# Kernel tuning notes

Hardware: AMD Instinct MI355X
Metric: run time of the kernel (lower is better)

## Reference

```python
import jax, jax.numpy as jnp
import numpy as np

B, N, DIM, HEADS, DIM_HEAD = 2, 2048, 1024, 16, 64
SCALE = DIM_HEAD ** -0.5


def setup_inputs() -> dict:
    key = jax.random.key(0)
    k1, k2, k3, k4, k5 = jax.random.split(key, 5)
    x = jax.random.normal(k1, (B, N, DIM), dtype=jnp.float32)
    causal_boundary_indices = jax.random.randint(k2, (B,), 0, N)
    # Parameters
    Wq = jax.random.normal(k3, (HEADS, DIM, DIM_HEAD), dtype=jnp.float32) * (DIM ** -0.5)
    Wkv = jax.random.normal(k4, (DIM, 2 * DIM_HEAD), dtype=jnp.float32) * (DIM ** -0.5)
    Wo = jax.random.normal(k5, (HEADS * DIM_HEAD, DIM), dtype=jnp.float32) * ((HEADS * DIM_HEAD) ** -0.5)
    return {"x": x, "Wq": Wq, "Wkv": Wkv, "Wo": Wo,
            "causal_boundary_indices": causal_boundary_indices}


def reference(x, Wq, Wkv, Wo, causal_boundary_indices):
    b, n, d = x.shape
    # Multi-query attention: per-head Q, single shared K/V head
    q = jnp.einsum('bnd,hde->bhne', x, Wq) * SCALE          # [b,h,n,dh]
    kv = x @ Wkv                                            # [b,n,2*dh]
    k, v = jnp.split(kv, 2, axis=-1)                        # [b,n,dh] each
    sim = jnp.einsum('bhid,bjd->bhij', q, k)                # [b,h,n,n]
    max_neg = -jnp.finfo(sim.dtype).max
    seq = jnp.arange(n)
    causal_mask = seq[None, :] > seq[:, None]               # [n,n] True = masked
    # positions j < boundary[b] are fully visible (prefix-LM); only j >= boundary obey causality
    mask_after = seq[None, None, None, :] >= causal_boundary_indices[:, None, None, None]
    mask = causal_mask[None, None, :, :] & mask_after       # [b,1,n,n]
    sim = jnp.where(mask, max_neg, sim)
    attn = jax.nn.softmax(sim, axis=-1)
    out = jnp.einsum('bhij,bjd->bhid', attn, v)             # [b,h,n,dh]
    out = out.transpose(0, 2, 1, 3).reshape(b, n, -1)       # [b,n,h*dh]
    return out @ Wo                                         # [b,n,d]
```

## Files before the change

kernel.cpp:

```cpp
#include <hip/hip_runtime.h>
#include <hip/hip_bf16.h>

typedef unsigned short ushort_t;
typedef unsigned int u32;
typedef __attribute__((ext_vector_type(8))) short bf16x8;
typedef __attribute__((ext_vector_type(4))) float f32x4;
typedef __attribute__((ext_vector_type(16))) float f32x16;
typedef __attribute__((ext_vector_type(2))) unsigned int u32x2;

#define L2E 1.44269504f

__device__ __forceinline__ ushort_t f2bf(float f) {
    union { __hip_bfloat16 b; ushort_t u; } c;
    c.b = __float2bfloat16(f);
    return c.u;
}

__device__ __forceinline__ f32x4 mfma16(bf16x8 a, bf16x8 b, f32x4 c) {
    return __builtin_amdgcn_mfma_f32_16x16x32_bf16(a, b, c, 0, 0, 0);
}

__device__ __forceinline__ f32x16 mfma32(bf16x8 a, bf16x8 b, f32x16 c) {
    return __builtin_amdgcn_mfma_f32_32x32x16_bf16(a, b, c, 0, 0, 0);
}

__device__ __forceinline__ u32 cvtpk(float lo, float hi) {
    u32 r;
    asm("v_cvt_pk_bf16_f32 %0, %1, %2" : "=v"(r) : "v"(lo), "v"(hi));
    return r;
}

__device__ __forceinline__ u32x2 pl32swap(u32 a, u32 b) {
#if __has_builtin(__builtin_amdgcn_permlane32_swap)
    auto r = __builtin_amdgcn_permlane32_swap((int)a, (int)b, false, false);
    return u32x2{(u32)r[0], (u32)r[1]};
#else
    u32 sa = (u32)__shfl_xor((int)a, 32);
    u32 sb = (u32)__shfl_xor((int)b, 32);
    int lane = threadIdx.x & 63;
    u32 d = (lane >= 32) ? sb : a;
    u32 s = (lane >= 32) ? b : sa;
    return u32x2{d, s};
#endif
}

__device__ __forceinline__ float swap32f(float x, int hi) {
    union { float f; u32 u; } c; c.f = x;
    u32x2 r = pl32swap(c.u, c.u);
    union { u32 u; float f; } o; o.u = hi ? r[0] : r[1];
    return o.f;
}

__device__ __forceinline__ void gload_lds16(const ushort_t* g, ushort_t* l) {
    __builtin_amdgcn_global_load_lds(
        (const __attribute__((address_space(1))) unsigned int*)g,
        (__attribute__((address_space(3))) unsigned int*)l, 16, 0, 0);
}


__device__ __forceinline__ int perm_off(int row, int k) {
    return (((row >> 6) & 1) * 8 + ((row >> 4) & 3) * 2 + ((k >> 5) & 1)) * 512
         + (row & 15) * 8 + ((k >> 3) & 3) * 128 + (k & 7);
}

__global__ __launch_bounds__(256)
void convert_kernel(const float* __restrict__ x, const float* __restrict__ Wq,
                    const float* __restrict__ Wkv, const float* __restrict__ Wo,
                    ushort_t* __restrict__ Xp, ushort_t* __restrict__ W1p,
                    ushort_t* __restrict__ Wop) {
    int idx = blockIdx.x * 256 + threadIdx.x;
    if (idx < 524288) {
        int row = idx >> 7, k = (idx & 127) << 3;
        const float* src = x + (size_t)row * 1024 + k;
        f32x4 a = *(const f32x4*)src, c2 = *(const f32x4*)(src + 4);
        union { u32 u[4]; bf16x8 v; } P;
        P.u[0] = cvtpk(a[0], a[1]);  P.u[1] = cvtpk(a[2], a[3]);
        P.u[2] = cvtpk(c2[0], c2[1]); P.u[3] = cvtpk(c2[2], c2[3]);
        size_t tile = (size_t)((row >> 7) * 16 + (k >> 6));
        *(bf16x8*)(Xp + tile * 8192 + perm_off(row, k)) = P.v;
        return;
    }
    idx -= 524288;
    if (idx < 294912) {
        int k = idx / 288, c = (idx % 288) * 4;
        f32x4 v;
        if (c < 1024) {
            v = *(const f32x4*)(Wq + ((size_t)((c >> 6) * 1024 + k)) * 64 + (c & 63));
            v *= 0.125f;
        } else {
            v = *(const f32x4*)(Wkv + (size_t)k * 128 + (c - 1024));
        }
        ushort_t* base = W1p + (size_t)((c >> 7) * 16 + (k >> 6)) * 8192;
#pragma unroll
        for (int i = 0; i < 4; i++) base[perm_off(c + i, k)] = f2bf(v[i]);
        return;
    }
    idx -= 294912;
    if (idx < 262144) {
        int k = idx >> 8, j = (idx & 255) * 4;
        f32x4 v = *(const f32x4*)(Wo + (size_t)k * 1024 + j);
        ushort_t* base = Wop + (size_t)((j >> 7) * 16 + (k >> 6)) * 8192;
#pragma unroll
        for (int i = 0; i < 4; i++) base[perm_off(j + i, k)] = f2bf(v[i]);
    }
}

template <int MODE>
__global__ __launch_bounds__(256, 3)
void gemmp(const ushort_t* __restrict__ Ap, const ushort_t* __restrict__ Bp,
           ushort_t* __restrict__ Cq, ushort_t* __restrict__ Ck,
           ushort_t* __restrict__ Cv, float* __restrict__ Cf) {
    __shared__ ushort_t smem[2][12288];
    const int tid = threadIdx.x, lane = tid & 63, w = tid >> 6;
    const int wm = w >> 1, wn = w & 1, l15 = lane & 15, g = lane >> 4;
    const int tm = blockIdx.x, tn = blockIdx.y;
    constexpr int KT = 16;

    f32x4 acc[2][4];
#pragma unroll
    for (int i = 0; i < 2; i++)
#pragma unroll
        for (int j = 0; j < 4; j++) acc[i][j] = (f32x4)(0.f);

    const ushort_t* Atile = Ap + ((size_t)(tm >> 1) * 16) * 8192 + (tm & 1) * 8 * 512;
    const ushort_t* Btile = Bp + ((size_t)tn * 16) * 8192;

    auto stage = [&](int buf, int kt) {
#pragma unroll
        for (int j = 0; j < 6; j++) {
            const int s = w * 6 + j;
            const ushort_t* gp = (s < 8)
                ? Atile + (size_t)kt * 8192 + s * 512 + lane * 8
                : Btile + (size_t)kt * 8192 + (s - 8) * 512 + lane * 8;
            gload_lds16(gp, &smem[buf][s * 512]);
        }
    };

    stage(0, 0);
    asm volatile("s_waitcnt vmcnt(0)" ::: "memory");
    __syncthreads();
    int cur = 0;
    for (int kt = 0; kt < KT; ++kt) {
        if (kt + 1 < KT) stage(cur ^ 1, kt + 1);
#pragma unroll
        for (int kc = 0; kc < 2; kc++) {
            bf16x8 af[2], bfr[4];
#pragma unroll
            for (int mi = 0; mi < 2; mi++)
                af[mi] = *(const bf16x8*)&smem[cur][((wm * 2 + mi) * 2 + kc) * 512 + lane * 8];
#pragma unroll
            for (int ni = 0; ni < 4; ni++)
                bfr[ni] = *(const bf16x8*)&smem[cur][(8 + wn * 8 + ni * 2 + kc) * 512 + lane * 8];
            __builtin_amdgcn_s_setprio(1);
#pragma unroll
            for (int mi = 0; mi < 2; mi++)
#pragma unroll
                for (int ni = 0; ni < 4; ni++)
                    acc[mi][ni] = mfma16(af[mi], bfr[ni], acc[mi][ni]);
            __builtin_amdgcn_s_setprio(0);
        }
        asm volatile("s_waitcnt vmcnt(0)" ::: "memory");
        __syncthreads();
        cur ^= 1;
    }

#pragma unroll
    for (int mi = 0; mi < 2; mi++)
#pragma unroll
        for (int ni = 0; ni < 4; ni++)
#pragma unroll
            for (int r = 0; r < 4; r++) {
                int row = tm * 64 + wm * 32 + mi * 16 + 4 * g + r;
                int col = tn * 128 + wn * 64 + ni * 16 + l15;
                float v = acc[mi][ni][r];
                if (MODE == 0) {
                    if (col < 1024) {
                        Cq[(size_t)row * 1024 + col] = f2bf(v);
                    } else if (col < 1088) {
                        int e = col - 1024;
                        int n = row & 2047, bb = row >> 11;
                        int t = n >> 6;
                        int idx = t * 4096 + (((n >> 5) & 1) * 4 + (e >> 4)) * 512 +
                                  (((e >> 3) & 1) * 32 + (n & 31)) * 8 + (e & 7);
                        Ck[(size_t)bb * 131072 + idx] = f2bf(v);
                    } else {
                        int d = col - 1088;
                        int n = row & 2047, bb = row >> 11;
                        int t = n >> 6;
                        int idx = t * 4096 + ((d >> 5) * 4 + ((n >> 4) & 3)) * 512 +
                                  (((n >> 3) & 1) * 32 + (d & 31)) * 8 + (n & 7);
                        Cv[(size_t)bb * 131072 + idx] = f2bf(v);
                    }
                } else {
                    Cf[(size_t)row * 1024 + col] = v;
                }
            }
}

__global__ __launch_bounds__(256, 2)
void attn32(const ushort_t* __restrict__ Qb, const ushort_t* __restrict__ Kt,
            const ushort_t* __restrict__ Vt2, ushort_t* __restrict__ Ob,
            const int* __restrict__ bnds) {
    __shared__ ushort_t sK[2][4096];
    __shared__ ushort_t sV[2][4096];
    const int tid = threadIdx.x;
    const int lane = tid & 63;
    const int w = tid >> 6;
    const int l31 = lane & 31;
    const int hi = lane >> 5;

    const int id = blockIdx.x;
    const int s = id & 255;
    const int flip = id >> 8;
    const int b = s >> 7;
    const int qt5 = (s >> 2) & 31;
    const int hg = s & 3;
    const int qt = flip ? 63 - qt5 : qt5;
    const int h = hg * 4 + w;
    const int bnd = bnds[b];
    const int qbase = qt * 32;
    const int q = qbase + l31;

    const ushort_t* Qp = Qb + ((size_t)(b * 2048 + q)) * 1024 + h * 64 + hi * 8;
    bf16x8 Qf[4];
#pragma unroll
    for (int kk = 0; kk < 4; kk++) Qf[kk] = *(const bf16x8*)(Qp + kk * 16);

    f32x16 oacc0 = (f32x16)(0.f), oacc1 = (f32x16)(0.f);
    float lsum = 0.f;
    const float mL = 8.0f * L2E;

    int wl = qbase + 31;
    if (bnd - 1 > wl) wl = bnd - 1;
    if (wl > 2047) wl = 2047;
    const int niter = (wl >> 6) + 1;

    const ushort_t* Kglob = Kt + (size_t)b * 131072;
    const ushort_t* Vglob = Vt2 + (size_t)b * 131072;

    auto stage = [&](int buf, int t) {
        if (w < 2) {
            const ushort_t* g = Kglob + (size_t)t * 4096 + (w * 4) * 512 + lane * 8;
            ushort_t* l = &sK[buf][(w * 4) * 512];
#pragma unroll
            for (int j = 0; j < 4; j++) gload_lds16(g + j * 512, l + j * 512);
        } else {
            const ushort_t* g = Vglob + (size_t)t * 4096 + ((w - 2) * 4) * 512 + lane * 8;
            ushort_t* l = &sV[buf][((w - 2) * 4) * 512];
#pragma unroll
            for (int j = 0; j < 4; j++) gload_lds16(g + j * 512, l + j * 512);
        }
    };

    stage(0, 0);
    asm volatile("s_waitcnt vmcnt(0)" ::: "memory");
    __syncthreads();

    int cur = 0;
    for (int it = 0; it < niter; ++it) {
        const int k0 = it * 64;
        if (it + 1 < niter) stage(cur ^ 1, it + 1);

        bf16x8 kfr[8];
#pragma unroll
        for (int r = 0; r < 8; r++)
            kfr[r] = *(const bf16x8*)&sK[cur][r * 512 + lane * 8];
        f32x16 s0 = (f32x16)(0.f), s1 = (f32x16)(0.f);
        __builtin_amdgcn_s_setprio(1);
#pragma unroll
        for (int kk = 0; kk < 4; kk++) {
            s0 = mfma32(kfr[kk], Qf[kk], s0);
            s1 = mfma32(kfr[4 + kk], Qf[kk], s1);
        }
        __builtin_amdgcn_s_setprio(0);

        const bool fullvis = (k0 + 63 <= qbase) || (k0 + 63 < bnd);
        if (!fullvis) {
#pragma unroll
            for (int r = 0; r < 16; r++) {
                int key0 = k0 + (r & 3) + 8 * (r >> 2) + 4 * hi;
                if (key0 > q && key0 >= bnd) s0[r] = -3e38f;
                int key1 = key0 + 32;
                if (key1 > q && key1 >= bnd) s1[r] = -3e38f;
            }
        }

        bf16x8 vfr[8];
#pragma unroll
        for (int r = 0; r < 8; r++)
            vfr[r] = *(const bf16x8*)&sV[cur][r * 512 + lane * 8];

        __builtin_amdgcn_s_setprio(1);
#pragma unroll
        for (int c = 0; c < 4; c++) {
            float p0, p1, p2, p3, p4, p5, p6, p7;
            {
                const f32x16& sc = (c < 2) ? s0 : s1;
                const int base = (c & 1) * 8;
                p0 = __builtin_amdgcn_exp2f(sc[base + 0] * L2E - mL);
                p1 = __builtin_amdgcn_exp2f(sc[base + 1] * L2E - mL);
                p2 = __builtin_amdgcn_exp2f(sc[base + 2] * L2E - mL);
                p3 = __builtin_amdgcn_exp2f(sc[base + 3] * L2E - mL);
                p4 = __builtin_amdgcn_exp2f(sc[base + 4] * L2E - mL);
                p5 = __builtin_amdgcn_exp2f(sc[base + 5] * L2E - mL);
                p6 = __builtin_amdgcn_exp2f(sc[base + 6] * L2E - mL);
                p7 = __builtin_amdgcn_exp2f(sc[base + 7] * L2E - mL);
            }
            lsum += ((p0 + p1) + (p2 + p3)) + ((p4 + p5) + (p6 + p7));
            u32 a0 = cvtpk(p0, p1);
            u32 c0 = cvtpk(p2, p3);
            u32 b0 = cvtpk(p4, p5);
            u32 d0 = cvtpk(p6, p7);
            u32x2 r02 = pl32swap(a0, b0);
            u32x2 r13 = pl32swap(c0, d0);
            union { u32 u[4]; bf16x8 v; } P;
            P.u[0] = r02[0]; P.u[1] = r13[0]; P.u[2] = r02[1]; P.u[3] = r13[1];
            oacc0 = mfma32(vfr[c], P.v, oacc0);
            oacc1 = mfma32(vfr[4 + c], P.v, oacc1);
        }
        __builtin_amdgcn_s_setprio(0);

        asm volatile("s_waitcnt vmcnt(0)" ::: "memory");
        __syncthreads();
        cur ^= 1;
    }

    const float ltot = lsum + swap32f(lsum, hi);
    const float li = 1.f / ltot;

    const int rowO = b * 2048 + q;
    const int segbase = ((rowO >> 6) & 1) * 8 + ((rowO >> 4) & 3) * 2;
    ushort_t* ObT = Ob + ((size_t)(rowO >> 7) * 16 + h) * 8192 + (rowO & 15) * 8 + 4 * hi;
#pragma unroll
    for (int dh = 0; dh < 2; dh++)
#pragma unroll
        for (int rq = 0; rq < 4; rq++) {
            union { ushort_t s[4]; u32x2 u; } st;
#pragma unroll
            for (int j = 0; j < 4; j++) {
                float v = (dh == 0 ? oacc0[4 * rq + j] : oacc1[4 * rq + j]) * li;
                st.s[j] = f2bf(v);
            }
            *(u32x2*)(ObT + (segbase + dh) * 512 + rq * 128) = st.u;
        }
}

extern "C" void kernel_launch(void* const* d_in, const int* in_sizes, int n_in,
                              void* d_out, int out_size, void* d_ws, size_t ws_size,
                              hipStream_t stream) {
    const float* x   = (const float*)d_in[0];
    const float* Wq  = (const float*)d_in[1];
    const float* Wkv = (const float*)d_in[2];
    const float* Wo  = (const float*)d_in[3];
    const int* bnds  = (const int*)d_in[4];
    char* ws = (char*)d_ws;
    ushort_t* Xbf  = (ushort_t*)(ws);
    ushort_t* W1bt = (ushort_t*)(ws + 8388608);
    ushort_t* Wobt = (ushort_t*)(ws + 10747904);
    ushort_t* Qb   = (ushort_t*)(ws + 12845056);
    ushort_t* Kb   = (ushort_t*)(ws + 21233664);
    ushort_t* Vt   = (ushort_t*)(ws + 21757952);
    ushort_t* Ob   = (ushort_t*)(ws + 22282240);
    float* out = (float*)d_out;

    convert_kernel<<<dim3(4224), dim3(256), 0, stream>>>(x, Wq, Wkv, Wo, Xbf, W1bt, Wobt);
    gemmp<0><<<dim3(64, 9), dim3(256), 0, stream>>>(Xbf, W1bt, Qb, Kb, Vt, (float*)nullptr);
    attn32<<<dim3(512), dim3(256), 0, stream>>>(Qb, Kb, Vt, Ob, bnds);
    gemmp<1><<<dim3(64, 8), dim3(256), 0, stream>>>(Ob, Wobt, (ushort_t*)nullptr,
                                                    (ushort_t*)nullptr, (ushort_t*)nullptr, out);
}
```

Baseline: 93.08 us.

## Process two K/V tiles per loop round to halve barriers and deepen staging

The attention loop now stages and processes two 64-key tiles per round, doubling the LDS buffers for K and V, with each wave loading a whole tile. The goal is to halve the number of __syncthreads/vmcnt waits per key and give the scheduler more independent MFMA and exp work to interleave. In exchange LDS use doubles to 64KB per block, which may limit occupancy at the requested 2 blocks per CU. Register pressure also rises from holding two score tiles at once, and V fragments are now read inside the chunk loop.

```diff
diff --git a/kernel.cpp b/kernel.cpp
--- a/kernel.cpp
+++ b/kernel.cpp
@@ -201,8 +201,8 @@
 void attn32(const ushort_t* __restrict__ Qb, const ushort_t* __restrict__ Kt,
             const ushort_t* __restrict__ Vt2, ushort_t* __restrict__ Ob,
             const int* __restrict__ bnds) {
-    __shared__ ushort_t sK[2][4096];
-    __shared__ ushort_t sV[2][4096];
+    __shared__ ushort_t sK[2][2][4096];
+    __shared__ ushort_t sV[2][2][4096];
     const int tid = threadIdx.x;
     const int lane = tid & 63;
     const int w = tid >> 6;
@@ -234,46 +234,21 @@
     if (bnd - 1 > wl) wl = bnd - 1;
     if (wl > 2047) wl = 2047;
     const int niter = (wl >> 6) + 1;
+    const int nrounds = (niter + 1) >> 1;
 
     const ushort_t* Kglob = Kt + (size_t)b * 131072;
     const ushort_t* Vglob = Vt2 + (size_t)b * 131072;
 
-    auto stage = [&](int buf, int t) {
-        if (w < 2) {
-            const ushort_t* g = Kglob + (size_t)t * 4096 + (w * 4) * 512 + lane * 8;
-            ushort_t* l = &sK[buf][(w * 4) * 512];
-#pragma unroll
-            for (int j = 0; j < 4; j++) gload_lds16(g + j * 512, l + j * 512);
-        } else {
-            const ushort_t* g = Vglob + (size_t)t * 4096 + ((w - 2) * 4) * 512 + lane * 8;
-            ushort_t* l = &sV[buf][((w - 2) * 4) * 512];
-#pragma unroll
-            for (int j = 0; j < 4; j++) gload_lds16(g + j * 512, l + j * 512);
-        }
+    const int stp = w & 1;
+    const ushort_t* sgbase = ((w >> 1) ? Vglob : Kglob) + (size_t)lane * 8;
+    auto stage = [&](int buf, int r) {
+        const ushort_t* g = sgbase + (size_t)(2 * r + stp) * 4096;
+        ushort_t* l = (w >> 1) ? &sV[buf][stp][0] : &sK[buf][stp][0];
+#pragma unroll
+        for (int j = 0; j < 8; j++) gload_lds16(g + j * 512, l + j * 512);
     };
 
-    stage(0, 0);
-    asm volatile("s_waitcnt vmcnt(0)" ::: "memory");
-    __syncthreads();
-
-    int cur = 0;
-    for (int it = 0; it < niter; ++it) {
-        const int k0 = it * 64;
-        if (it + 1 < niter) stage(cur ^ 1, it + 1);
-
-        bf16x8 kfr[8];
-#pragma unroll
-        for (int r = 0; r < 8; r++)
-            kfr[r] = *(const bf16x8*)&sK[cur][r * 512 + lane * 8];
-        f32x16 s0 = (f32x16)(0.f), s1 = (f32x16)(0.f);
-        __builtin_amdgcn_s_setprio(1);
-#pragma unroll
-        for (int kk = 0; kk < 4; kk++) {
-            s0 = mfma32(kfr[kk], Qf[kk], s0);
-            s1 = mfma32(kfr[4 + kk], Qf[kk], s1);
-        }
-        __builtin_amdgcn_s_setprio(0);
-
+    auto mask_tile = [&](int k0, f32x16& s0, f32x16& s1) {
         const bool fullvis = (k0 + 63 <= qbase) || (k0 + 63 < bnd);
         if (!fullvis) {
 #pragma unroll
@@ -284,39 +259,84 @@
                 if (key1 > q && key1 >= bnd) s1[r] = -3e38f;
             }
         }
-
-        bf16x8 vfr[8];
-#pragma unroll
-        for (int r = 0; r < 8; r++)
-            vfr[r] = *(const bf16x8*)&sV[cur][r * 512 + lane * 8];
+    };
+
+    auto chunk = [&](const f32x16& s0, const f32x16& s1, const ushort_t* vb, int c) {
+        float p0, p1, p2, p3, p4, p5, p6, p7;
+        {
+            const f32x16& sc = (c < 2) ? s0 : s1;
+            const int base = (c & 1) * 8;
+            p0 = __builtin_amdgcn_exp2f(sc[base + 0] * L2E - mL);
+            p1 = __builtin_amdgcn_exp2f(sc[base + 1] * L2E - mL);
+            p2 = __builtin_amdgcn_exp2f(sc[base + 2] * L2E - mL);
+            p3 = __builtin_amdgcn_exp2f(sc[base + 3] * L2E - mL);
+            p4 = __builtin_amdgcn_exp2f(sc[base + 4] * L2E - mL);
+            p5 = __builtin_amdgcn_exp2f(sc[base + 5] * L2E - mL);
+            p6 = __builtin_amdgcn_exp2f(sc[base + 6] * L2E - mL);
+            p7 = __builtin_amdgcn_exp2f(sc[base + 7] * L2E - mL);
+        }
+        lsum += ((p0 + p1) + (p2 + p3)) + ((p4 + p5) + (p6 + p7));
+        u32 a0 = cvtpk(p0, p1);
+        u32 c0 = cvtpk(p2, p3);
+        u32 b0 = cvtpk(p4, p5);
+        u32 d0 = cvtpk(p6, p7);
+        u32x2 r02 = pl32swap(a0, b0);
+        u32x2 r13 = pl32swap(c0, d0);
+        union { u32 u[4]; bf16x8 v; } P;
+        P.u[0] = r02[0]; P.u[1] = r13[0]; P.u[2] = r02[1]; P.u[3] = r13[1];
+        bf16x8 vf0 = *(const bf16x8*)&vb[c * 512 + lane * 8];
+        bf16x8 vf1 = *(const bf16x8*)&vb[(4 + c) * 512 + lane * 8];
+        oacc0 = mfma32(vf0, P.v, oacc0);
+        oacc1 = mfma32(vf1, P.v, oacc1);
+    };
+
+    stage(0, 0);
+    asm volatile("s_waitcnt vmcnt(0)" ::: "memory");
+    __syncthreads();
+
+    int cur = 0;
+    for (int r = 0; r < nrounds; ++r) {
+        if (r + 1 < nrounds) stage(cur ^ 1, r + 1);
+        const int t0 = 2 * r, t1 = 2 * r + 1;
+        const bool has1 = (t1 < niter);
+
+        f32x16 sa0 = (f32x16)(0.f), sa1 = (f32x16)(0.f);
+        f32x16 sb0 = (f32x16)(0.f), sb1 = (f32x16)(0.f);
+        {
+            bf16x8 kf[8];
+#pragma unroll
+            for (int r8 = 0; r8 < 8; r8++)
+                kf[r8] = *(const bf16x8*)&sK[cur][0][r8 * 512 + lane * 8];
+            __builtin_amdgcn_s_setprio(1);
+#pragma unroll
+            for (int kk = 0; kk < 4; kk++) {
+                sa0 = mfma32(kf[kk], Qf[kk], sa0);
+                sa1 = mfma32(kf[4 + kk], Qf[kk], sa1);
+            }
+            __builtin_amdgcn_s_setprio(0);
+        }
+        if (has1) {
+            bf16x8 kg[8];
+#pragma unroll
+            for (int r8 = 0; r8 < 8; r8++)
+                kg[r8] = *(const bf16x8*)&sK[cur][1][r8 * 512 + lane * 8];
+            __builtin_amdgcn_s_setprio(1);
+#pragma unroll
+            for (int kk = 0; kk < 4; kk++) {
+                sb0 = mfma32(kg[kk], Qf[kk], sb0);
+                sb1 = mfma32(kg[4 + kk], Qf[kk], sb1);
+            }
+            __builtin_amdgcn_s_setprio(0);
+        }
+
+        mask_tile(t0 * 64, sa0, sa1);
+        if (has1) mask_tile(t1 * 64, sb0, sb1);
 
         __builtin_amdgcn_s_setprio(1);
 #pragma unroll
         for (int c = 0; c < 4; c++) {
-            float p0, p1, p2, p3, p4, p5, p6, p7;
-            {
-                const f32x16& sc = (c < 2) ? s0 : s1;
-                const int base = (c & 1) * 8;
-                p0 = __builtin_amdgcn_exp2f(sc[base + 0] * L2E - mL);
-                p1 = __builtin_amdgcn_exp2f(sc[base + 1] * L2E - mL);
-                p2 = __builtin_amdgcn_exp2f(sc[base + 2] * L2E - mL);
-                p3 = __builtin_amdgcn_exp2f(sc[base + 3] * L2E - mL);
-                p4 = __builtin_amdgcn_exp2f(sc[base + 4] * L2E - mL);
-                p5 = __builtin_amdgcn_exp2f(sc[base + 5] * L2E - mL);
-                p6 = __builtin_amdgcn_exp2f(sc[base + 6] * L2E - mL);
-                p7 = __builtin_amdgcn_exp2f(sc[base + 7] * L2E - mL);
-            }
-            lsum += ((p0 + p1) + (p2 + p3)) + ((p4 + p5) + (p6 + p7));
-            u32 a0 = cvtpk(p0, p1);
-            u32 c0 = cvtpk(p2, p3);
-            u32 b0 = cvtpk(p4, p5);
-            u32 d0 = cvtpk(p6, p7);
-            u32x2 r02 = pl32swap(a0, b0);
-            u32x2 r13 = pl32swap(c0, d0);
-            union { u32 u[4]; bf16x8 v; } P;
-            P.u[0] = r02[0]; P.u[1] = r13[0]; P.u[2] = r02[1]; P.u[3] = r13[1];
-            oacc0 = mfma32(vfr[c], P.v, oacc0);
-            oacc1 = mfma32(vfr[4 + c], P.v, oacc1);
+            chunk(sa0, sa1, &sV[cur][0][0], c);
+            if (has1) chunk(sb0, sb1, &sV[cur][1][0], c);
         }
         __builtin_amdgcn_s_setprio(0);
 
```

After: 93.60 us. No clear change (+0.6%).

## Switch attention kernel to 16x16 MFMA tiles with 16-query blocks

Applied to the files above, without the earlier changes.

Rewrites the attention kernel to use 16x16x32 MFMA with 16 queries per wave instead of 32x32x16 with 32 queries. The K/V layouts written by the projection GEMM change to match, and the grid doubles to 1024 blocks with occupancy hint raised to 4. The aim is more parallelism and finer causal work skipping, since each block stops closer to its diagonal. The cost is twice the K/V reloads across blocks, and the P fragments are now exchanged with __shfl (LDS-routed) instead of permlane32 swaps.

```diff
diff --git a/kernel.cpp b/kernel.cpp
--- a/kernel.cpp
+++ b/kernel.cpp
@@ -20,35 +20,10 @@
     return __builtin_amdgcn_mfma_f32_16x16x32_bf16(a, b, c, 0, 0, 0);
 }
 
-__device__ __forceinline__ f32x16 mfma32(bf16x8 a, bf16x8 b, f32x16 c) {
-    return __builtin_amdgcn_mfma_f32_32x32x16_bf16(a, b, c, 0, 0, 0);
-}
-
 __device__ __forceinline__ u32 cvtpk(float lo, float hi) {
     u32 r;
     asm("v_cvt_pk_bf16_f32 %0, %1, %2" : "=v"(r) : "v"(lo), "v"(hi));
     return r;
-}
-
-__device__ __forceinline__ u32x2 pl32swap(u32 a, u32 b) {
-#if __has_builtin(__builtin_amdgcn_permlane32_swap)
-    auto r = __builtin_amdgcn_permlane32_swap((int)a, (int)b, false, false);
-    return u32x2{(u32)r[0], (u32)r[1]};
-#else
-    u32 sa = (u32)__shfl_xor((int)a, 32);
-    u32 sb = (u32)__shfl_xor((int)b, 32);
-    int lane = threadIdx.x & 63;
-    u32 d = (lane >= 32) ? sb : a;
-    u32 s = (lane >= 32) ? b : sa;
-    return u32x2{d, s};
-#endif
-}
-
-__device__ __forceinline__ float swap32f(float x, int hi) {
-    union { float f; u32 u; } c; c.f = x;
-    u32x2 r = pl32swap(c.u, c.u);
-    union { u32 u; float f; } o; o.u = hi ? r[0] : r[1];
-    return o.f;
 }
 
 __device__ __forceinline__ void gload_lds16(const ushort_t* g, ushort_t* l) {
@@ -180,15 +155,15 @@
                         int e = col - 1024;
                         int n = row & 2047, bb = row >> 11;
                         int t = n >> 6;
-                        int idx = t * 4096 + (((n >> 5) & 1) * 4 + (e >> 4)) * 512 +
-                                  (((e >> 3) & 1) * 32 + (n & 31)) * 8 + (e & 7);
+                        int idx = t * 4096 + ((((n >> 4) & 3) * 2 + (e >> 5))) * 512 +
+                                  (n & 15) * 8 + ((e >> 3) & 3) * 128 + (e & 7);
                         Ck[(size_t)bb * 131072 + idx] = f2bf(v);
                     } else {
                         int d = col - 1088;
                         int n = row & 2047, bb = row >> 11;
                         int t = n >> 6;
-                        int idx = t * 4096 + ((d >> 5) * 4 + ((n >> 4) & 3)) * 512 +
-                                  (((n >> 3) & 1) * 32 + (d & 31)) * 8 + (n & 7);
+                        int idx = t * 4096 + (((d >> 4) * 2 + ((n >> 5) & 1))) * 512 +
+                                  (d & 15) * 8 + ((n >> 3) & 3) * 128 + (n & 7);
                         Cv[(size_t)bb * 131072 + idx] = f2bf(v);
                     }
                 } else {
@@ -197,8 +172,8 @@
             }
 }
 
-__global__ __launch_bounds__(256, 2)
-void attn32(const ushort_t* __restrict__ Qb, const ushort_t* __restrict__ Kt,
+__global__ __launch_bounds__(256, 4)
+void attn16(const ushort_t* __restrict__ Qb, const ushort_t* __restrict__ Kt,
             const ushort_t* __restrict__ Vt2, ushort_t* __restrict__ Ob,
             const int* __restrict__ bnds) {
     __shared__ ushort_t sK[2][4096];
@@ -206,31 +181,30 @@
     const int tid = threadIdx.x;
     const int lane = tid & 63;
     const int w = tid >> 6;
-    const int l31 = lane & 31;
-    const int hi = lane >> 5;
+    const int q16 = lane & 15;
+    const int g = lane >> 4;
 
     const int id = blockIdx.x;
-    const int s = id & 255;
-    const int flip = id >> 8;
-    const int b = s >> 7;
-    const int qt5 = (s >> 2) & 31;
-    const int hg = s & 3;
-    const int qt = flip ? 63 - qt5 : qt5;
+    const int hg = id & 3;
+    const int qt6 = (id >> 2) & 63;
+    const int b = (id >> 8) & 1;
+    const int flip = id >> 9;
+    const int qt = flip ? 127 - qt6 : qt6;
     const int h = hg * 4 + w;
     const int bnd = bnds[b];
-    const int qbase = qt * 32;
-    const int q = qbase + l31;
-
-    const ushort_t* Qp = Qb + ((size_t)(b * 2048 + q)) * 1024 + h * 64 + hi * 8;
-    bf16x8 Qf[4];
-#pragma unroll
-    for (int kk = 0; kk < 4; kk++) Qf[kk] = *(const bf16x8*)(Qp + kk * 16);
-
-    f32x16 oacc0 = (f32x16)(0.f), oacc1 = (f32x16)(0.f);
+    const int qbase = qt * 16;
+
+    const ushort_t* Qp = Qb + ((size_t)(b * 2048 + qbase + q16)) * 1024 + h * 64 + g * 8;
+    bf16x8 Qf0 = *(const bf16x8*)(Qp);
+    bf16x8 Qf1 = *(const bf16x8*)(Qp + 32);
+
+    f32x4 oacc[4];
+#pragma unroll
+    for (int i = 0; i < 4; i++) oacc[i] = (f32x4)(0.f);
     float lsum = 0.f;
     const float mL = 8.0f * L2E;
 
-    int wl = qbase + 31;
+    int wl = qbase + 15;
     if (bnd - 1 > wl) wl = bnd - 1;
     if (wl > 2047) wl = 2047;
     const int niter = (wl >> 6) + 1;
@@ -240,15 +214,15 @@
 
     auto stage = [&](int buf, int t) {
         if (w < 2) {
-            const ushort_t* g = Kglob + (size_t)t * 4096 + (w * 4) * 512 + lane * 8;
+            const ushort_t* gp = Kglob + (size_t)t * 4096 + (w * 4) * 512 + lane * 8;
             ushort_t* l = &sK[buf][(w * 4) * 512];
 #pragma unroll
-            for (int j = 0; j < 4; j++) gload_lds16(g + j * 512, l + j * 512);
+            for (int j = 0; j < 4; j++) gload_lds16(gp + j * 512, l + j * 512);
         } else {
-            const ushort_t* g = Vglob + (size_t)t * 4096 + ((w - 2) * 4) * 512 + lane * 8;
+            const ushort_t* gp = Vglob + (size_t)t * 4096 + ((w - 2) * 4) * 512 + lane * 8;
             ushort_t* l = &sV[buf][((w - 2) * 4) * 512];
 #pragma unroll
-            for (int j = 0; j < 4; j++) gload_lds16(g + j * 512, l + j * 512);
+            for (int j = 0; j < 4; j++) gload_lds16(gp + j * 512, l + j * 512);
         }
     };
 
@@ -261,62 +235,59 @@
         const int k0 = it * 64;
         if (it + 1 < niter) stage(cur ^ 1, it + 1);
 
-        bf16x8 kfr[8];
-#pragma unroll
-        for (int r = 0; r < 8; r++)
-            kfr[r] = *(const bf16x8*)&sK[cur][r * 512 + lane * 8];
-        f32x16 s0 = (f32x16)(0.f), s1 = (f32x16)(0.f);
+        f32x4 sT[4];
         __builtin_amdgcn_s_setprio(1);
 #pragma unroll
-        for (int kk = 0; kk < 4; kk++) {
-            s0 = mfma32(kfr[kk], Qf[kk], s0);
-            s1 = mfma32(kfr[4 + kk], Qf[kk], s1);
+        for (int kg = 0; kg < 4; kg++) {
+            bf16x8 kf0 = *(const bf16x8*)&sK[cur][(kg * 2 + 0) * 512 + lane * 8];
+            bf16x8 kf1 = *(const bf16x8*)&sK[cur][(kg * 2 + 1) * 512 + lane * 8];
+            f32x4 t = (f32x4)(0.f);
+            t = mfma16(kf0, Qf0, t);
+            t = mfma16(kf1, Qf1, t);
+            sT[kg] = t;
         }
         __builtin_amdgcn_s_setprio(0);
 
         const bool fullvis = (k0 + 63 <= qbase) || (k0 + 63 < bnd);
         if (!fullvis) {
-#pragma unroll
-            for (int r = 0; r < 16; r++) {
-                int key0 = k0 + (r & 3) + 8 * (r >> 2) + 4 * hi;
-                if (key0 > q && key0 >= bnd) s0[r] = -3e38f;
-                int key1 = key0 + 32;
-                if (key1 > q && key1 >= bnd) s1[r] = -3e38f;
+            const int q = qbase + q16;
+#pragma unroll
+            for (int kg = 0; kg < 4; kg++)
+#pragma unroll
+                for (int r = 0; r < 4; r++) {
+                    int key = k0 + kg * 16 + 4 * g + r;
+                    if (key > q && key >= bnd) sT[kg][r] = -3e38f;
+                }
+        }
+
+        u32 pk[4][2];
+#pragma unroll
+        for (int kg = 0; kg < 4; kg++) {
+            float p0 = __builtin_amdgcn_exp2f(sT[kg][0] * L2E - mL);
+            float p1 = __builtin_amdgcn_exp2f(sT[kg][1] * L2E - mL);
+            float p2 = __builtin_amdgcn_exp2f(sT[kg][2] * L2E - mL);
+            float p3 = __builtin_amdgcn_exp2f(sT[kg][3] * L2E - mL);
+            lsum += (p0 + p1) + (p2 + p3);
+            pk[kg][0] = cvtpk(p0, p1);
+            pk[kg][1] = cvtpk(p2, p3);
+        }
+
+        __builtin_amdgcn_s_setprio(1);
+#pragma unroll
+        for (int kh = 0; kh < 2; kh++) {
+            union { u32 u[4]; bf16x8 v; } PU;
+#pragma unroll
+            for (int w2 = 0; w2 < 4; w2++) {
+                int srcLane = q16 + 16 * (2 * (g & 1) + (w2 >> 1));
+                u32 lo = (u32)__shfl((int)pk[kh * 2 + 0][w2 & 1], srcLane);
+                u32 hi = (u32)__shfl((int)pk[kh * 2 + 1][w2 & 1], srcLane);
+                PU.u[w2] = (g < 2) ? lo : hi;
             }
-        }
-
-        bf16x8 vfr[8];
-#pragma unroll
-        for (int r = 0; r < 8; r++)
-            vfr[r] = *(const bf16x8*)&sV[cur][r * 512 + lane * 8];
-
-        __builtin_amdgcn_s_setprio(1);
-#pragma unroll
-        for (int c = 0; c < 4; c++) {
-            float p0, p1, p2, p3, p4, p5, p6, p7;
-            {
-                const f32x16& sc = (c < 2) ? s0 : s1;
-                const int base = (c & 1) * 8;
-                p0 = __builtin_amdgcn_exp2f(sc[base + 0] * L2E - mL);
-                p1 = __builtin_amdgcn_exp2f(sc[base + 1] * L2E - mL);
-                p2 = __builtin_amdgcn_exp2f(sc[base + 2] * L2E - mL);
-                p3 = __builtin_amdgcn_exp2f(sc[base + 3] * L2E - mL);
-                p4 = __builtin_amdgcn_exp2f(sc[base + 4] * L2E - mL);
-                p5 = __builtin_amdgcn_exp2f(sc[base + 5] * L2E - mL);
-                p6 = __builtin_amdgcn_exp2f(sc[base + 6] * L2E - mL);
-                p7 = __builtin_amdgcn_exp2f(sc[base + 7] * L2E - mL);
+#pragma unroll
+            for (int dg = 0; dg < 4; dg++) {
+                bf16x8 vf = *(const bf16x8*)&sV[cur][(dg * 2 + kh) * 512 + lane * 8];
+                oacc[dg] = mfma16(vf, PU.v, oacc[dg]);
             }
-            lsum += ((p0 + p1) + (p2 + p3)) + ((p4 + p5) + (p6 + p7));
-            u32 a0 = cvtpk(p0, p1);
-            u32 c0 = cvtpk(p2, p3);
-            u32 b0 = cvtpk(p4, p5);
-            u32 d0 = cvtpk(p6, p7);
-            u32x2 r02 = pl32swap(a0, b0);
-            u32x2 r13 = pl32swap(c0, d0);
-            union { u32 u[4]; bf16x8 v; } P;
-            P.u[0] = r02[0]; P.u[1] = r13[0]; P.u[2] = r02[1]; P.u[3] = r13[1];
-            oacc0 = mfma32(vfr[c], P.v, oacc0);
-            oacc1 = mfma32(vfr[4 + c], P.v, oacc1);
         }
         __builtin_amdgcn_s_setprio(0);
 
@@ -325,24 +296,21 @@
         cur ^= 1;
     }
 
-    const float ltot = lsum + swap32f(lsum, hi);
-    const float li = 1.f / ltot;
-
-    const int rowO = b * 2048 + q;
-    const int segbase = ((rowO >> 6) & 1) * 8 + ((rowO >> 4) & 3) * 2;
-    ushort_t* ObT = Ob + ((size_t)(rowO >> 7) * 16 + h) * 8192 + (rowO & 15) * 8 + 4 * hi;
-#pragma unroll
-    for (int dh = 0; dh < 2; dh++)
-#pragma unroll
-        for (int rq = 0; rq < 4; rq++) {
-            union { ushort_t s[4]; u32x2 u; } st;
-#pragma unroll
-            for (int j = 0; j < 4; j++) {
-                float v = (dh == 0 ? oacc0[4 * rq + j] : oacc1[4 * rq + j]) * li;
-                st.s[j] = f2bf(v);
-            }
-            *(u32x2*)(ObT + (segbase + dh) * 512 + rq * 128) = st.u;
-        }
+    lsum += __shfl_xor(lsum, 16);
+    lsum += __shfl_xor(lsum, 32);
+    const float li = 1.f / lsum;
+
+    const int row0 = b * 2048 + qbase + q16;
+    const int segbase = ((row0 >> 6) & 1) * 8 + ((row0 >> 4) & 3) * 2;
+    ushort_t* ObT = Ob + ((size_t)(row0 >> 7) * 16 + h) * 8192 + (row0 & 15) * 8
+                  + (g >> 1) * 128 + 4 * (g & 1);
+#pragma unroll
+    for (int dg = 0; dg < 4; dg++) {
+        union { ushort_t s[4]; u32x2 u; } st;
+#pragma unroll
+        for (int r = 0; r < 4; r++) st.s[r] = f2bf(oacc[dg][r] * li);
+        *(u32x2*)(ObT + (size_t)(segbase + (dg >> 1)) * 512 + (dg & 1) * 256) = st.u;
+    }
 }
 
 extern "C" void kernel_launch(void* const* d_in, const int* in_sizes, int n_in,
@@ -365,7 +333,7 @@
 
     convert_kernel<<<dim3(4224), dim3(256), 0, stream>>>(x, Wq, Wkv, Wo, Xbf, W1bt, Wobt);
     gemmp<0><<<dim3(64, 9), dim3(256), 0, stream>>>(Xbf, W1bt, Qb, Kb, Vt, (float*)nullptr);
-    attn32<<<dim3(512), dim3(256), 0, stream>>>(Qb, Kb, Vt, Ob, bnds);
+    attn16<<<dim3(1024), dim3(256), 0, stream>>>(Qb, Kb, Vt, Ob, bnds);
     gemmp<1><<<dim3(64, 8), dim3(256), 0, stream>>>(Ob, Wobt, (ushort_t*)nullptr,
                                                     (ushort_t*)nullptr, (ushort_t*)nullptr, out);
 }
```

Result: slower. 108.2 us (+16.2%).

## Give each wave private K/V LDS buffers and drop block barriers in attention

Applied to the files above, without the earlier changes.

The attention kernel now has each wave stage its own copy of the K and V tiles into a per-wave LDS region, using 32-key tiles instead of 64. That lets it replace the block-wide __syncthreads with per-wave vmcnt waits, and the K/V layouts written by the projection GEMM are reindexed to match the 32-key tiles. The goal is to remove barrier stalls and let waves run independently, at the cost of fetching the same K/V four times per block, twice as many loop iterations, and four times the LDS per block, which may lower occupancy.

```diff
diff --git a/kernel.cpp b/kernel.cpp
--- a/kernel.cpp
+++ b/kernel.cpp
@@ -179,16 +179,14 @@
                     } else if (col < 1088) {
                         int e = col - 1024;
                         int n = row & 2047, bb = row >> 11;
-                        int t = n >> 6;
-                        int idx = t * 4096 + (((n >> 5) & 1) * 4 + (e >> 4)) * 512 +
-                                  (((e >> 3) & 1) * 32 + (n & 31)) * 8 + (e & 7);
+                        int idx = (n >> 5) * 2048 + (e >> 4) * 512 +
+                                  ((e >> 3) & 1) * 256 + (n & 31) * 8 + (e & 7);
                         Ck[(size_t)bb * 131072 + idx] = f2bf(v);
                     } else {
                         int d = col - 1088;
                         int n = row & 2047, bb = row >> 11;
-                        int t = n >> 6;
-                        int idx = t * 4096 + ((d >> 5) * 4 + ((n >> 4) & 3)) * 512 +
-                                  (((n >> 3) & 1) * 32 + (d & 31)) * 8 + (n & 7);
+                        int idx = (n >> 5) * 2048 + ((d >> 5) * 2 + ((n >> 4) & 1)) * 512 +
+                                  ((n >> 3) & 1) * 256 + (d & 31) * 8 + (n & 7);
                         Cv[(size_t)bb * 131072 + idx] = f2bf(v);
                     }
                 } else {
@@ -198,11 +196,10 @@
 }
 
 __global__ __launch_bounds__(256, 2)
-void attn32(const ushort_t* __restrict__ Qb, const ushort_t* __restrict__ Kt,
+void attnbf(const ushort_t* __restrict__ Qb, const ushort_t* __restrict__ Kt,
             const ushort_t* __restrict__ Vt2, ushort_t* __restrict__ Ob,
             const int* __restrict__ bnds) {
-    __shared__ ushort_t sK[2][4096];
-    __shared__ ushort_t sV[2][4096];
+    __shared__ ushort_t sKV[4][2][4096];
     const int tid = threadIdx.x;
     const int lane = tid & 63;
     const int w = tid >> 6;
@@ -233,95 +230,78 @@
     int wl = qbase + 31;
     if (bnd - 1 > wl) wl = bnd - 1;
     if (wl > 2047) wl = 2047;
-    const int niter = (wl >> 6) + 1;
-
-    const ushort_t* Kglob = Kt + (size_t)b * 131072;
-    const ushort_t* Vglob = Vt2 + (size_t)b * 131072;
+    const int niter = (wl >> 5) + 1;
+
+    const ushort_t* Kglob = Kt + (size_t)b * 131072 + lane * 8;
+    const ushort_t* Vglob = Vt2 + (size_t)b * 131072 + lane * 8;
 
     auto stage = [&](int buf, int t) {
-        if (w < 2) {
-            const ushort_t* g = Kglob + (size_t)t * 4096 + (w * 4) * 512 + lane * 8;
-            ushort_t* l = &sK[buf][(w * 4) * 512];
-#pragma unroll
-            for (int j = 0; j < 4; j++) gload_lds16(g + j * 512, l + j * 512);
-        } else {
-            const ushort_t* g = Vglob + (size_t)t * 4096 + ((w - 2) * 4) * 512 + lane * 8;
-            ushort_t* l = &sV[buf][((w - 2) * 4) * 512];
-#pragma unroll
-            for (int j = 0; j < 4; j++) gload_lds16(g + j * 512, l + j * 512);
+        const ushort_t* gk = Kglob + (size_t)t * 2048;
+        const ushort_t* gv = Vglob + (size_t)t * 2048;
+        ushort_t* lk = &sKV[w][buf][0];
+        ushort_t* lv = &sKV[w][buf][2048];
+#pragma unroll
+        for (int s8 = 0; s8 < 4; s8++) {
+            gload_lds16(gk + s8 * 512, lk + s8 * 512);
+            gload_lds16(gv + s8 * 512, lv + s8 * 512);
         }
     };
 
     stage(0, 0);
-    asm volatile("s_waitcnt vmcnt(0)" ::: "memory");
-    __syncthreads();
-
     int cur = 0;
     for (int it = 0; it < niter; ++it) {
-        const int k0 = it * 64;
-        if (it + 1 < niter) stage(cur ^ 1, it + 1);
-
-        bf16x8 kfr[8];
-#pragma unroll
-        for (int r = 0; r < 8; r++)
-            kfr[r] = *(const bf16x8*)&sK[cur][r * 512 + lane * 8];
-        f32x16 s0 = (f32x16)(0.f), s1 = (f32x16)(0.f);
+        if (it + 1 < niter) {
+            stage(cur ^ 1, it + 1);
+            asm volatile("s_waitcnt vmcnt(8)" ::: "memory");
+        } else {
+            asm volatile("s_waitcnt vmcnt(0)" ::: "memory");
+        }
+        const int k0 = it * 32;
+        const ushort_t* kb = &sKV[w][cur][0];
+        const ushort_t* vb = &sKV[w][cur][2048];
+
+        bf16x8 kf[4];
+#pragma unroll
+        for (int kk = 0; kk < 4; kk++)
+            kf[kk] = *(const bf16x8*)&kb[kk * 512 + lane * 8];
+        f32x16 s0 = (f32x16)(0.f);
         __builtin_amdgcn_s_setprio(1);
 #pragma unroll
-        for (int kk = 0; kk < 4; kk++) {
-            s0 = mfma32(kfr[kk], Qf[kk], s0);
-            s1 = mfma32(kfr[4 + kk], Qf[kk], s1);
-        }
+        for (int kk = 0; kk < 4; kk++) s0 = mfma32(kf[kk], Qf[kk], s0);
         __builtin_amdgcn_s_setprio(0);
 
-        const bool fullvis = (k0 + 63 <= qbase) || (k0 + 63 < bnd);
+        const bool fullvis = (k0 + 31 <= qbase) || (k0 + 31 < bnd);
         if (!fullvis) {
 #pragma unroll
             for (int r = 0; r < 16; r++) {
-                int key0 = k0 + (r & 3) + 8 * (r >> 2) + 4 * hi;
-                if (key0 > q && key0 >= bnd) s0[r] = -3e38f;
-                int key1 = key0 + 32;
-                if (key1 > q && key1 >= bnd) s1[r] = -3e38f;
+                int key = k0 + (r & 3) + 8 * (r >> 2) + 4 * hi;
+                if (key > q && key >= bnd) s0[r] = -3e38f;
             }
         }
 
-        bf16x8 vfr[8];
-#pragma unroll
-        for (int r = 0; r < 8; r++)
-            vfr[r] = *(const bf16x8*)&sV[cur][r * 512 + lane * 8];
+        u32 pk[8];
+#pragma unroll
+        for (int i = 0; i < 8; i++) {
+            float pa = __builtin_amdgcn_exp2f(s0[2 * i] * L2E - mL);
+            float pb = __builtin_amdgcn_exp2f(s0[2 * i + 1] * L2E - mL);
+            lsum += pa + pb;
+            pk[i] = cvtpk(pa, pb);
+        }
 
         __builtin_amdgcn_s_setprio(1);
 #pragma unroll
-        for (int c = 0; c < 4; c++) {
-            float p0, p1, p2, p3, p4, p5, p6, p7;
-            {
-                const f32x16& sc = (c < 2) ? s0 : s1;
-                const int base = (c & 1) * 8;
-                p0 = __builtin_amdgcn_exp2f(sc[base + 0] * L2E - mL);
-                p1 = __builtin_amdgcn_exp2f(sc[base + 1] * L2E - mL);
-                p2 = __builtin_amdgcn_exp2f(sc[base + 2] * L2E - mL);
-                p3 = __builtin_amdgcn_exp2f(sc[base + 3] * L2E - mL);
-                p4 = __builtin_amdgcn_exp2f(sc[base + 4] * L2E - mL);
-                p5 = __builtin_amdgcn_exp2f(sc[base + 5] * L2E - mL);
-                p6 = __builtin_amdgcn_exp2f(sc[base + 6] * L2E - mL);
-                p7 = __builtin_amdgcn_exp2f(sc[base + 7] * L2E - mL);
-            }
-            lsum += ((p0 + p1) + (p2 + p3)) + ((p4 + p5) + (p6 + p7));
-            u32 a0 = cvtpk(p0, p1);
-            u32 c0 = cvtpk(p2, p3);
-            u32 b0 = cvtpk(p4, p5);
-            u32 d0 = cvtpk(p6, p7);
-            u32x2 r02 = pl32swap(a0, b0);
-            u32x2 r13 = pl32swap(c0, d0);
+        for (int ks = 0; ks < 2; ks++) {
+            u32x2 w02 = pl32swap(pk[4 * ks + 0], pk[4 * ks + 2]);
+            u32x2 w13 = pl32swap(pk[4 * ks + 1], pk[4 * ks + 3]);
             union { u32 u[4]; bf16x8 v; } P;
-            P.u[0] = r02[0]; P.u[1] = r13[0]; P.u[2] = r02[1]; P.u[3] = r13[1];
-            oacc0 = mfma32(vfr[c], P.v, oacc0);
-            oacc1 = mfma32(vfr[4 + c], P.v, oacc1);
+            P.u[0] = w02[0]; P.u[1] = w13[0]; P.u[2] = w02[1]; P.u[3] = w13[1];
+            bf16x8 vf0 = *(const bf16x8*)&vb[(0 * 2 + ks) * 512 + lane * 8];
+            bf16x8 vf1 = *(const bf16x8*)&vb[(1 * 2 + ks) * 512 + lane * 8];
+            oacc0 = mfma32(vf0, P.v, oacc0);
+            oacc1 = mfma32(vf1, P.v, oacc1);
         }
         __builtin_amdgcn_s_setprio(0);
 
-        asm volatile("s_waitcnt vmcnt(0)" ::: "memory");
-        __syncthreads();
         cur ^= 1;
     }
 
@@ -365,7 +345,7 @@
 
     convert_kernel<<<dim3(4224), dim3(256), 0, stream>>>(x, Wq, Wkv, Wo, Xbf, W1bt, Wobt);
     gemmp<0><<<dim3(64, 9), dim3(256), 0, stream>>>(Xbf, W1bt, Qb, Kb, Vt, (float*)nullptr);
-    attn32<<<dim3(512), dim3(256), 0, stream>>>(Qb, Kb, Vt, Ob, bnds);
+    attnbf<<<dim3(512), dim3(256), 0, stream>>>(Qb, Kb, Vt, Ob, bnds);
     gemmp<1><<<dim3(64, 8), dim3(256), 0, stream>>>(Ob, Wobt, (ushort_t*)nullptr,
                                                     (ushort_t*)nullptr, (ushort_t*)nullptr, out);
 }
```

After: 102.7 us. +10.3%, slower.
